# Kernel tuning notes

Measured on AMD Instinct MI355X. Metric: run time of the kernel, lower is better.

The kernel has to match this reference:

```python
import jax, jax.numpy as jnp
import numpy as np

N = 100000   # nodes
E = 1600000  # edges (avg degree 16)
D = 128      # in_dim == hidden_dim
L = 3        # num_layers
LN_EPS = 1e-5


def setup_inputs() -> dict:
    key = jax.random.key(0)
    ks = jax.random.split(key, 4)
    x = jax.random.normal(ks[0], (N, D), dtype=jnp.float32)
    edge_index = jax.random.randint(ks[1], (2, E), 0, N, dtype=jnp.int32)
    s = 1.0 / np.sqrt(D)
    W1 = jax.random.normal(ks[2], (L, D, D), dtype=jnp.float32) * s
    b1 = jnp.zeros((L, D), jnp.float32)
    W2 = jax.random.normal(ks[3], (L, D, D), dtype=jnp.float32) * s
    b2 = jnp.zeros((L, D), jnp.float32)
    gamma = jnp.ones((L, D), jnp.float32)
    beta = jnp.zeros((L, D), jnp.float32)
    return dict(x=x, edge_index=edge_index, W1=W1, b1=b1, W2=W2, b2=b2,
                gamma=gamma, beta=beta)


def _layer_norm(h, g, b):
    mu = jnp.mean(h, axis=-1, keepdims=True)
    var = jnp.mean((h - mu) ** 2, axis=-1, keepdims=True)
    return (h - mu) * jax.lax.rsqrt(var + LN_EPS) * g + b


def reference(x, edge_index, W1, b1, W2, b2, gamma, beta):
    # PyG GINConv (eps=0): mlp(x + sum_{j in N(i)} x_j), messages flow src->dst.
    src, dst = edge_index[0], edge_index[1]
    h = x
    for l in range(L):
        agg = jax.ops.segment_sum(h[src], dst, num_segments=N)  # [N, D]
        z = h + agg                                              # (1+eps)*x + agg, eps=0
        z = jnp.maximum(z @ W1[l] + b1[l], 0.0) @ W2[l] + b2[l]  # 2-layer MLP
        h = jnp.maximum(_layer_norm(z, gamma[l], beta[l]), 0.0)  # LayerNorm + ReLU
        # dropout p=0.0 (eval): identity
    return h
```

## Files before the change

### kernel.cpp

```cpp
#include <hip/hip_runtime.h>

#define NN 100000
#define EE 1600000
#define DD 128
#define LL 3

typedef float f32x4 __attribute__((ext_vector_type(4)));
typedef _Float16 f16x8 __attribute__((ext_vector_type(8)));
typedef _Float16 f16x2 __attribute__((ext_vector_type(2)));
typedef unsigned short u16;
typedef unsigned int u32;
typedef u16 u16x8 __attribute__((ext_vector_type(8)));

#define NBUCK ((NN + 255) / 256)
#define CHUNK 16384
#define NCHUNK ((EE + CHUNK - 1) / CHUNK)
#define PADMAX 1792

__device__ __forceinline__ u16 f2h_bits(float f) {
    _Float16 h = (_Float16)f;
    return __builtin_bit_cast(u16, h);
}
__device__ __forceinline__ f16x2 bc16x2(u32 v) {
    return __builtin_bit_cast(f16x2, v);
}
__device__ __forceinline__ u32 f22h(float x, float y) {
    return (u32)f2h_bits(x) | ((u32)f2h_bits(y) << 16);
}


__global__ __launch_bounds__(1024) void csr_hist(const int* __restrict__ dst,
                                                 int* __restrict__ hist_g) {
    __shared__ int h[NBUCK];
    int t = threadIdx.x, c = blockIdx.x;
    for (int i = t; i < NBUCK; i += 1024) h[i] = 0;
    __syncthreads();
    int base = c * CHUNK;
    #pragma unroll
    for (int i = 0; i < CHUNK / 1024; ++i) {
        int e = base + t + i * 1024;
        if (e < EE) atomicAdd(&h[dst[e] >> 8], 1);
    }
    __syncthreads();
    for (int i = t; i < NBUCK; i += 1024) hist_g[i * NCHUNK + c] = h[i];
}

__global__ __launch_bounds__(512) void csr_scan(int* __restrict__ hist_g,
                                                int* __restrict__ bbase) {
    __shared__ int tot[512];
    int t = threadIdx.x;
    int sum = 0;
    if (t < NBUCK) {
        int* p = hist_g + t * NCHUNK;
        for (int c = 0; c < NCHUNK; ++c) { int v = p[c]; p[c] = sum; sum += v; }
    }
    tot[t] = sum; __syncthreads();
    for (int off = 1; off < 512; off <<= 1) {
        int u = (t >= off) ? tot[t - off] : 0;
        __syncthreads();
        tot[t] += u;
        __syncthreads();
    }
    int base = tot[t] - sum;
    if (t < NBUCK) {
        bbase[t] = base;
        int* p = hist_g + t * NCHUNK;
        for (int c = 0; c < NCHUNK; ++c) p[c] += base;
    }
    if (t == 0) bbase[NBUCK] = EE;
}

__global__ __launch_bounds__(1024) void csr_scatter(const int* __restrict__ src,
                                                    const int* __restrict__ dst,
                                                    const int* __restrict__ hist_g,
                                                    u32* __restrict__ rec) {
    __shared__ int cur[NBUCK];
    int t = threadIdx.x, c = blockIdx.x;
    for (int i = t; i < NBUCK; i += 1024) cur[i] = hist_g[i * NCHUNK + c];
    __syncthreads();
    int base = c * CHUNK;
    #pragma unroll
    for (int i = 0; i < CHUNK / 1024; ++i) {
        int e = base + t + i * 1024;
        if (e < EE) {
            int d = dst[e];
            int slot = atomicAdd(&cur[d >> 8], 1);
            rec[slot] = (u32)src[e] | ((u32)(d & 255) << 17);
        }
    }
}

__global__ __launch_bounds__(256) void csr_finalize(const u32* __restrict__ rec,
                                                    const int* __restrict__ bbase,
                                                    int* __restrict__ rbeg,
                                                    int* __restrict__ rpend,
                                                    int* __restrict__ col) {
    __shared__ int cur[256];
    __shared__ int sc[256];
    int b = blockIdx.x, t = threadIdx.x;
    int base = bbase[b], tot = bbase[b + 1] - base;
    int pbase = base + b * PADMAX;
    sc[t] = 0; __syncthreads();
    for (int r = t; r < tot; r += 256) atomicAdd(&sc[rec[base + r] >> 17], 1);
    __syncthreads();
    int cnt = sc[t];
    int pcnt = (cnt + 7) & ~7;
    sc[t] = pcnt; __syncthreads();
    for (int off = 1; off < 256; off <<= 1) {
        int u = (t >= off) ? sc[t - off] : 0;
        __syncthreads();
        sc[t] += u;
        __syncthreads();
    }
    int mybeg = pbase + sc[t] - pcnt;
    cur[t] = mybeg;
    int nid = b * 256 + t;
    if (nid < NN) { rbeg[nid] = mybeg; rpend[nid] = mybeg + pcnt; }
    for (int k = cnt; k < pcnt; ++k) col[mybeg + k] = NN;
    __syncthreads();
    for (int r = t; r < tot; r += 256) {
        u32 rc = rec[base + r];
        int slot = atomicAdd(&cur[rc >> 17], 1);
        col[slot] = (int)(rc & 0x1FFFFu);
    }
}


__global__ void cvt_kernel(const float* __restrict__ x, u32* __restrict__ h) {
    int i = blockIdx.x * blockDim.x + threadIdx.x;
    if (i < NN * 32) {
        float4 v = ((const float4*)x)[i];
        h[i * 2]     = f22h(v.x, v.y);
        h[i * 2 + 1] = f22h(v.z, v.w);
    }
}


__global__ __launch_bounds__(256) void wconv_kernel(const float* __restrict__ W1,
                                                    const float* __restrict__ W2,
                                                    u16* __restrict__ img) {
    int tt = blockIdx.x * 256 + threadIdx.x;
    if (tt >= 6 * 2048) return;
    int m = tt >> 11;
    int q = tt & 2047;
    int l = m >> 1;
    const float* W = ((m & 1) ? W2 : W1) + (size_t)l * DD * DD;
    int c = q & 127;
    int k0 = (q >> 7) << 3;
    u16x8 t;
    #pragma unroll
    for (int j = 0; j < 8; ++j) t[j] = f2h_bits(W[(k0 + j) * 128 + c]);
    u32 off = ((((u32)c << 7) + k0) << 1) ^ (((u32)c & 7) << 4);
    *(u16x8*)((unsigned char*)img + (size_t)m * 32768 + off) = t;
}


__global__ __launch_bounds__(256) void agg16_kernel(
    const u32* __restrict__ h, const int* __restrict__ rbeg,
    const int* __restrict__ rpend, const int* __restrict__ col,
    u32* __restrict__ z) {
    int node = blockIdx.x * 4 + (threadIdx.x >> 6);
    int c = threadIdx.x & 63;
    const u32* hp = h + c;
    f16x2 self = bc16x2(hp[(size_t)node * 64]);
    float accx = (float)self[0], accy = (float)self[1];
    int beg = rbeg[node], end = rpend[node];
    for (int j = beg; j < end; j += 8) {
        u32 v[8];
        #pragma unroll
        for (int q = 0; q < 8; ++q) v[q] = hp[(size_t)col[j + q] * 64];
        f16x2 s0 = bc16x2(v[0]) + bc16x2(v[1]);
        f16x2 s1 = bc16x2(v[2]) + bc16x2(v[3]);
        f16x2 s2 = bc16x2(v[4]) + bc16x2(v[5]);
        f16x2 s3 = bc16x2(v[6]) + bc16x2(v[7]);
        s0 = s0 + s1; s2 = s2 + s3; s0 = s0 + s2;
        accx += (float)s0[0]; accy += (float)s0[1];
    }
    z[(size_t)node * 64 + c] = f22h(accx, accy);
}


__device__ __forceinline__ void stage_img(const u32* __restrict__ img,
                                          unsigned char* lds, int tid) {
    #pragma unroll
    for (int i = 0; i < 8; ++i) {
        int b = tid * 16 + i * 4096;
        *(uint4*)(lds + b) = *(const uint4*)((const unsigned char*)img + b);
    }
}

__global__ __launch_bounds__(256) void mlp_kernel(
    const u16* __restrict__ z16, const u32* __restrict__ img1,
    const float* __restrict__ b1v, const u32* __restrict__ img2,
    const float* __restrict__ b2v, const float* __restrict__ gam,
    const float* __restrict__ bet, u16* __restrict__ h16out,
    float* __restrict__ f32out)
{
    __shared__ __align__(16) unsigned char lds[49152];
    const int tid = threadIdx.x;
    const int lane = tid & 63;
    const int w = tid >> 6;
    const int rl = lane & 15;
    const int kg = lane >> 4;
    const int tile = blockIdx.x * 64;
    const int r0 = tile + w * 16;

    stage_img(img1, lds, tid);

    int zrow = r0 + rl; if (zrow > NN - 1) zrow = NN - 1;
    const u16* zp = z16 + (size_t)zrow * 128;
    f16x8 afr[4];
    #pragma unroll
    for (int kt = 0; kt < 4; ++kt)
        afr[kt] = *(const f16x8*)(zp + kt * 32 + kg * 8);
    __syncthreads();

    #pragma unroll
    for (int nt = 0; nt < 8; ++nt) {
        f32x4 acc = {0.f, 0.f, 0.f, 0.f};
        int c = nt * 16 + rl;
        #pragma unroll
        for (int kt = 0; kt < 4; ++kt) {
            int kb = kt * 32 + kg * 8;
            u32 off = ((((u32)c << 7) + kb) << 1) ^ (((u32)c & 7) << 4);
            f16x8 b = *(const f16x8*)(lds + off);
            acc = __builtin_amdgcn_mfma_f32_16x16x32_f16(afr[kt], b, acc, 0, 0, 0);
        }
        float bias = b1v[c];
        #pragma unroll
        for (int r = 0; r < 4; ++r) {
            float v = acc[r] + bias;
            v = v > 0.f ? v : 0.f;
            int fullrow = w * 16 + kg * 4 + r;
            u32 hoff = 32768u + (((((u32)fullrow << 7) + c) << 1) ^ (((u32)fullrow & 7) << 4));
            *(u16*)(lds + hoff) = f2h_bits(v);
        }
    }

    __syncthreads();
    stage_img(img2, lds, tid);

    f16x8 afr2[4];
    int hrow = w * 16 + rl;
    #pragma unroll
    for (int kt = 0; kt < 4; ++kt) {
        int kb = kt * 32 + kg * 8;
        u32 off = 32768u + (((((u32)hrow << 7) + kb) << 1) ^ (((u32)hrow & 7) << 4));
        afr2[kt] = *(const f16x8*)(lds + off);
    }
    __syncthreads();

    f32x4 acc2[8];
    #pragma unroll
    for (int nt = 0; nt < 8; ++nt) {
        f32x4 acc = {0.f, 0.f, 0.f, 0.f};
        int c = nt * 16 + rl;
        #pragma unroll
        for (int kt = 0; kt < 4; ++kt) {
            int kb = kt * 32 + kg * 8;
            u32 off = ((((u32)c << 7) + kb) << 1) ^ (((u32)c & 7) << 4);
            f16x8 b = *(const f16x8*)(lds + off);
            acc = __builtin_amdgcn_mfma_f32_16x16x32_f16(afr2[kt], b, acc, 0, 0, 0);
        }
        float bias = b2v[c];
        acc[0] += bias; acc[1] += bias; acc[2] += bias; acc[3] += bias;
        acc2[nt] = acc;
    }

    float gamv[8], betv[8];
    #pragma unroll
    for (int nt = 0; nt < 8; ++nt) { gamv[nt] = gam[nt * 16 + rl]; betv[nt] = bet[nt * 16 + rl]; }
    #pragma unroll
    for (int r = 0; r < 4; ++r) {
        float s1 = 0.f, s2 = 0.f;
        #pragma unroll
        for (int nt = 0; nt < 8; ++nt) { float v = acc2[nt][r]; s1 += v; s2 += v * v; }
        #pragma unroll
        for (int m = 1; m < 16; m <<= 1) {
            s1 += __shfl_xor(s1, m, 64);
            s2 += __shfl_xor(s2, m, 64);
        }
        float mu = s1 * (1.f / 128.f);
        float var = s2 * (1.f / 128.f) - mu * mu;
        float rstd = rsqrtf(var + 1e-5f);
        int fullrow = r0 + kg * 4 + r;
        if (fullrow < NN) {
            #pragma unroll
            for (int nt = 0; nt < 8; ++nt) {
                float v = (acc2[nt][r] - mu) * rstd * gamv[nt] + betv[nt];
                v = v > 0.f ? v : 0.f;
                if (h16out) h16out[(size_t)fullrow * 128 + nt * 16 + rl] = f2h_bits(v);
                if (f32out) f32out[(size_t)fullrow * 128 + nt * 16 + rl] = v;
            }
        }
    }
}


extern "C" void kernel_launch(void* const* d_in, const int* in_sizes, int n_in,
                              void* d_out, int out_size, void* d_ws, size_t ws_size,
                              hipStream_t stream) {
    const float* x     = (const float*)d_in[0];
    const int*   ei    = (const int*)d_in[1];
    const float* W1    = (const float*)d_in[2];
    const float* b1    = (const float*)d_in[3];
    const float* W2    = (const float*)d_in[4];
    const float* b2    = (const float*)d_in[5];
    const float* gamma = (const float*)d_in[6];
    const float* beta  = (const float*)d_in[7];
    float* out = (float*)d_out;

    const int* src = ei;
    const int* dst = ei + EE;

    unsigned char* ws = (unsigned char*)d_ws;
    size_t off = 0;
    int* hist_g  = (int*)(ws + off); off += (size_t)NBUCK * NCHUNK * 4;
    int* bbase   = (int*)(ws + off); off += (size_t)(NBUCK + 1) * 4;
    int* rbeg    = (int*)(ws + off); off += (size_t)NN * 4;
    int* rpend   = (int*)(ws + off); off += (size_t)NN * 4; off = (off + 255) & ~(size_t)255;
    u16* wimg    = (u16*)(ws + off); off += (size_t)6 * 16384 * 2; off = (off + 255) & ~(size_t)255;
    u32* rec     = (u32*)(ws + off); off += (size_t)EE * 4; off = (off + 255) & ~(size_t)255;
    int* colv    = (int*)(ws + off); off += ((size_t)EE + (size_t)NBUCK * PADMAX + 64) * 4;
    off = (off + 255) & ~(size_t)255;
    u32* h16a    = (u32*)(ws + off); off += (size_t)(NN + 1) * 64 * 4;
    u32* h16b    = (u32*)(ws + off); off += (size_t)(NN + 1) * 64 * 4;
    u32* z16     = (u32*)(ws + off); off += (size_t)NN * 64 * 4;

    csr_hist<<<NCHUNK, 1024, 0, stream>>>(dst, hist_g);
    csr_scan<<<1, 512, 0, stream>>>(hist_g, bbase);
    csr_scatter<<<NCHUNK, 1024, 0, stream>>>(src, dst, hist_g, rec);
    csr_finalize<<<NBUCK, 256, 0, stream>>>(rec, bbase, rbeg, rpend, colv);
    wconv_kernel<<<48, 256, 0, stream>>>(W1, W2, wimg);
    cvt_kernel<<<(NN * 32 + 255) / 256, 256, 0, stream>>>(x, h16a);
    hipMemsetAsync(h16a + (size_t)NN * 64, 0, 256, stream);
    hipMemsetAsync(h16b + (size_t)NN * 64, 0, 256, stream);

    const u32* hin = h16a;
    u32* hnext = h16b;
    for (int l = 0; l < LL; ++l) {
        agg16_kernel<<<NN / 4, 256, 0, stream>>>(hin, rbeg, rpend, colv, z16);
        mlp_kernel<<<(NN + 63) / 64, 256, 0, stream>>>(
            (const u16*)z16,
            (const u32*)(wimg + (size_t)(2 * l) * 16384), b1 + l * DD,
            (const u32*)(wimg + (size_t)(2 * l + 1) * 16384), b2 + l * DD,
            gamma + l * DD, beta + l * DD,
            (l < LL - 1) ? (u16*)hnext : (u16*)nullptr,
            (l == LL - 1) ? out : (float*)nullptr);
        hin = hnext;
        hnext = (hnext == h16a) ? h16b : h16a;
    }
}
```

Measured before the change: 336.5 us.

## Parallelize CSR scan, pad rows to 4, widen MLP blocks, fold memsets into convert

Replaces the single-block serial scan over the chunk histograms with a per-bucket parallel scan plus a small bucket scan, and adds the bucket base inside the scatter kernel. Row padding drops from 8 to 4 slots, with a 4-wide tail in aggregation, which cuts the gather of dummy zero rows. The MLP kernel moves to 512 threads over 128 rows per block so the weight image staged in LDS serves more rows. The two sentinel-row memsets are folded into the convert kernel to save launches. The larger LDS footprint and block size may lower occupancy.

```diff
diff --git a/kernel.cpp b/kernel.cpp
--- a/kernel.cpp
+++ b/kernel.cpp
@@ -15,7 +15,7 @@
 #define NBUCK ((NN + 255) / 256)
 #define CHUNK 16384
 #define NCHUNK ((EE + CHUNK - 1) / CHUNK)
-#define PADMAX 1792
+#define PADMAX 768
 
 __device__ __forceinline__ u16 f2h_bits(float f) {
     _Float16 h = (_Float16)f;
@@ -45,38 +45,46 @@
     for (int i = t; i < NBUCK; i += 1024) hist_g[i * NCHUNK + c] = h[i];
 }
 
-__global__ __launch_bounds__(512) void csr_scan(int* __restrict__ hist_g,
-                                                int* __restrict__ bbase) {
-    __shared__ int tot[512];
+__global__ __launch_bounds__(128) void csr_scanA(int* __restrict__ hist_g,
+                                                 int* __restrict__ btot) {
+    __shared__ int sh[128];
+    int b = blockIdx.x, t = threadIdx.x;
+    int v = (t < NCHUNK) ? hist_g[b * NCHUNK + t] : 0;
+    sh[t] = v; __syncthreads();
+    for (int off = 1; off < 128; off <<= 1) {
+        int u = (t >= off) ? sh[t - off] : 0;
+        __syncthreads();
+        sh[t] += u;
+        __syncthreads();
+    }
+    if (t < NCHUNK) hist_g[b * NCHUNK + t] = sh[t] - v;
+    if (t == 127) btot[b] = sh[127];
+}
+
+__global__ __launch_bounds__(512) void csr_scanB(const int* __restrict__ btot,
+                                                 int* __restrict__ bbase) {
+    __shared__ int sh[512];
     int t = threadIdx.x;
-    int sum = 0;
-    if (t < NBUCK) {
-        int* p = hist_g + t * NCHUNK;
-        for (int c = 0; c < NCHUNK; ++c) { int v = p[c]; p[c] = sum; sum += v; }
-    }
-    tot[t] = sum; __syncthreads();
+    int v = (t < NBUCK) ? btot[t] : 0;
+    sh[t] = v; __syncthreads();
     for (int off = 1; off < 512; off <<= 1) {
-        int u = (t >= off) ? tot[t - off] : 0;
-        __syncthreads();
-        tot[t] += u;
-        __syncthreads();
-    }
-    int base = tot[t] - sum;
-    if (t < NBUCK) {
-        bbase[t] = base;
-        int* p = hist_g + t * NCHUNK;
-        for (int c = 0; c < NCHUNK; ++c) p[c] += base;
-    }
+        int u = (t >= off) ? sh[t - off] : 0;
+        __syncthreads();
+        sh[t] += u;
+        __syncthreads();
+    }
+    if (t < NBUCK) bbase[t] = sh[t] - v;
     if (t == 0) bbase[NBUCK] = EE;
 }
 
 __global__ __launch_bounds__(1024) void csr_scatter(const int* __restrict__ src,
                                                     const int* __restrict__ dst,
                                                     const int* __restrict__ hist_g,
+                                                    const int* __restrict__ bbase,
                                                     u32* __restrict__ rec) {
     __shared__ int cur[NBUCK];
     int t = threadIdx.x, c = blockIdx.x;
-    for (int i = t; i < NBUCK; i += 1024) cur[i] = hist_g[i * NCHUNK + c];
+    for (int i = t; i < NBUCK; i += 1024) cur[i] = bbase[i] + hist_g[i * NCHUNK + c];
     __syncthreads();
     int base = c * CHUNK;
     #pragma unroll
@@ -104,7 +112,7 @@
     for (int r = t; r < tot; r += 256) atomicAdd(&sc[rec[base + r] >> 17], 1);
     __syncthreads();
     int cnt = sc[t];
-    int pcnt = (cnt + 7) & ~7;
+    int pcnt = (cnt + 3) & ~3;
     sc[t] = pcnt; __syncthreads();
     for (int off = 1; off < 256; off <<= 1) {
         int u = (t >= off) ? sc[t - off] : 0;
@@ -126,12 +134,19 @@
 }
 
 
-__global__ void cvt_kernel(const float* __restrict__ x, u32* __restrict__ h) {
+__global__ void cvt_kernel(const float* __restrict__ x, u32* __restrict__ ha,
+                           u32* __restrict__ hb) {
     int i = blockIdx.x * blockDim.x + threadIdx.x;
     if (i < NN * 32) {
         float4 v = ((const float4*)x)[i];
-        h[i * 2]     = f22h(v.x, v.y);
-        h[i * 2 + 1] = f22h(v.z, v.w);
+        ha[i * 2]     = f22h(v.x, v.y);
+        ha[i * 2 + 1] = f22h(v.z, v.w);
+    } else {
+        int k = i - NN * 32;
+        if (k < 64) {
+            ha[(size_t)NN * 64 + k] = 0;
+            hb[(size_t)NN * 64 + k] = 0;
+        }
     }
 }
 
@@ -165,7 +180,8 @@
     f16x2 self = bc16x2(hp[(size_t)node * 64]);
     float accx = (float)self[0], accy = (float)self[1];
     int beg = rbeg[node], end = rpend[node];
-    for (int j = beg; j < end; j += 8) {
+    int j = beg;
+    for (; j + 8 <= end; j += 8) {
         u32 v[8];
         #pragma unroll
         for (int q = 0; q < 8; ++q) v[q] = hp[(size_t)col[j + q] * 64];
@@ -176,6 +192,16 @@
         s0 = s0 + s1; s2 = s2 + s3; s0 = s0 + s2;
         accx += (float)s0[0]; accy += (float)s0[1];
     }
+    if (j < end) {
+        u32 v0 = hp[(size_t)col[j] * 64];
+        u32 v1 = hp[(size_t)col[j + 1] * 64];
+        u32 v2 = hp[(size_t)col[j + 2] * 64];
+        u32 v3 = hp[(size_t)col[j + 3] * 64];
+        f16x2 t0 = bc16x2(v0) + bc16x2(v1);
+        f16x2 t1 = bc16x2(v2) + bc16x2(v3);
+        t0 = t0 + t1;
+        accx += (float)t0[0]; accy += (float)t0[1];
+    }
     z[(size_t)node * 64 + c] = f22h(accx, accy);
 }
 
@@ -183,26 +209,26 @@
 __device__ __forceinline__ void stage_img(const u32* __restrict__ img,
                                           unsigned char* lds, int tid) {
     #pragma unroll
-    for (int i = 0; i < 8; ++i) {
-        int b = tid * 16 + i * 4096;
+    for (int i = 0; i < 4; ++i) {
+        int b = tid * 16 + i * 8192;
         *(uint4*)(lds + b) = *(const uint4*)((const unsigned char*)img + b);
     }
 }
 
-__global__ __launch_bounds__(256) void mlp_kernel(
+__global__ __launch_bounds__(512) void mlp_kernel(
     const u16* __restrict__ z16, const u32* __restrict__ img1,
     const float* __restrict__ b1v, const u32* __restrict__ img2,
     const float* __restrict__ b2v, const float* __restrict__ gam,
     const float* __restrict__ bet, u16* __restrict__ h16out,
     float* __restrict__ f32out)
 {
-    __shared__ __align__(16) unsigned char lds[49152];
+    __shared__ __align__(16) unsigned char lds[65536];
     const int tid = threadIdx.x;
     const int lane = tid & 63;
     const int w = tid >> 6;
     const int rl = lane & 15;
     const int kg = lane >> 4;
-    const int tile = blockIdx.x * 64;
+    const int tile = blockIdx.x * 128;
     const int r0 = tile + w * 16;
 
     stage_img(img1, lds, tid);
@@ -316,6 +342,7 @@
     unsigned char* ws = (unsigned char*)d_ws;
     size_t off = 0;
     int* hist_g  = (int*)(ws + off); off += (size_t)NBUCK * NCHUNK * 4;
+    int* btot    = (int*)(ws + off); off += (size_t)(NBUCK + 1) * 4;
     int* bbase   = (int*)(ws + off); off += (size_t)(NBUCK + 1) * 4;
     int* rbeg    = (int*)(ws + off); off += (size_t)NN * 4;
     int* rpend   = (int*)(ws + off); off += (size_t)NN * 4; off = (off + 255) & ~(size_t)255;
@@ -328,19 +355,18 @@
     u32* z16     = (u32*)(ws + off); off += (size_t)NN * 64 * 4;
 
     csr_hist<<<NCHUNK, 1024, 0, stream>>>(dst, hist_g);
-    csr_scan<<<1, 512, 0, stream>>>(hist_g, bbase);
-    csr_scatter<<<NCHUNK, 1024, 0, stream>>>(src, dst, hist_g, rec);
+    csr_scanA<<<NBUCK, 128, 0, stream>>>(hist_g, btot);
+    csr_scanB<<<1, 512, 0, stream>>>(btot, bbase);
+    csr_scatter<<<NCHUNK, 1024, 0, stream>>>(src, dst, hist_g, bbase, rec);
     csr_finalize<<<NBUCK, 256, 0, stream>>>(rec, bbase, rbeg, rpend, colv);
     wconv_kernel<<<48, 256, 0, stream>>>(W1, W2, wimg);
-    cvt_kernel<<<(NN * 32 + 255) / 256, 256, 0, stream>>>(x, h16a);
-    hipMemsetAsync(h16a + (size_t)NN * 64, 0, 256, stream);
-    hipMemsetAsync(h16b + (size_t)NN * 64, 0, 256, stream);
+    cvt_kernel<<<NN * 32 / 256 + 1, 256, 0, stream>>>(x, h16a, h16b);
 
     const u32* hin = h16a;
     u32* hnext = h16b;
     for (int l = 0; l < LL; ++l) {
         agg16_kernel<<<NN / 4, 256, 0, stream>>>(hin, rbeg, rpend, colv, z16);
-        mlp_kernel<<<(NN + 63) / 64, 256, 0, stream>>>(
+        mlp_kernel<<<(NN + 127) / 128, 512, 0, stream>>>(
             (const u16*)z16,
             (const u32*)(wimg + (size_t)(2 * l) * 16384), b1 + l * DD,
             (const u32*)(wimg + (size_t)(2 * l + 1) * 16384), b2 + l * DD,
```

After: 311.3 us. 1.08x faster.
